# Performance work log

Hardware: AMD Instinct MI355X
Metric: run time of the kernel (lower is better)

Reference implementation:

```python
import jax, jax.numpy as jnp
import numpy as np

D_E = 100   # entity embedding dim
D_R = 100   # relation embedding dim
RANK = 40   # TR rank
N_ENT = 10000
N_REL = 50
B = 128
EPS = 1e-5  # torch BatchNorm1d default eps


def _bn(x, gamma, beta):
    # BatchNorm1d in training mode: biased batch statistics over the batch dim.
    mu = x.mean(axis=0)
    var = x.var(axis=0)  # ddof=0, matches torch normalization variance
    return gamma * (x - mu) * jax.lax.rsqrt(var + EPS) + beta


def _tr_to_tensor(f0, f1, f2, f3):
    # Tensor-ring reconstruction of W with ring trace; factors are [R, d, R].
    # Pairwise contraction keeps intermediates at [R, d, d, R] (256 MB max).
    A = jnp.einsum('aib,bjc->aijc', f0, f1)   # [R, d_r, d_e, R]
    C = jnp.einsum('ckd,dla->ckla', f2, f3)   # [R, d_e, d_e, R]
    return jnp.einsum('aijc,ckla->ijkl', A, C)  # [d_r, d_e, d_e, d_e]


def setup_inputs() -> dict:
    key = jax.random.key(0)
    ks = jax.random.split(key, 10)
    E_weight = 0.001 * jax.random.normal(ks[0], (N_ENT, D_E), dtype=jnp.float32)
    E_weight = E_weight.at[0].set(0.0)  # padding_idx=0
    R_weight = 0.001 * jax.random.normal(ks[1], (N_REL, D_R), dtype=jnp.float32)
    R_weight = R_weight.at[0].set(0.0)
    f0 = jax.random.normal(ks[2], (RANK, D_R, RANK), dtype=jnp.float32) * 0.05
    f1 = jax.random.normal(ks[3], (RANK, D_E, RANK), dtype=jnp.float32) * 0.05
    f2 = jax.random.normal(ks[4], (RANK, D_E, RANK), dtype=jnp.float32) * 0.05
    f3 = jax.random.normal(ks[5], (RANK, D_E, RANK), dtype=jnp.float32) * 0.05
    bnr_g = jnp.ones((D_R,), jnp.float32); bnr_b = jnp.zeros((D_R,), jnp.float32)
    bne_g = jnp.ones((D_E,), jnp.float32); bne_b = jnp.zeros((D_E,), jnp.float32)
    bnw_g = jnp.ones((D_E,), jnp.float32); bnw_b = jnp.zeros((D_E,), jnp.float32)
    r_idx = jax.random.randint(ks[6], (B,), 0, N_REL)
    e_idx1 = jax.random.randint(ks[7], (B,), 0, N_ENT)
    e_idx2 = jax.random.randint(ks[8], (B,), 0, N_ENT)
    return {
        'E_weight': E_weight, 'R_weight': R_weight,
        'f0': f0, 'f1': f1, 'f2': f2, 'f3': f3,
        'bnr_g': bnr_g, 'bnr_b': bnr_b,
        'bne_g': bne_g, 'bne_b': bne_b,
        'bnw_g': bnw_g, 'bnw_b': bnw_b,
        'r_idx': r_idx, 'e_idx1': e_idx1, 'e_idx2': e_idx2,
        'miss_ent_domain': 2,
    }


def reference(E_weight, R_weight, f0, f1, f2, f3,
              bnr_g, bnr_b, bne_g, bne_b, bnw_g, bnw_b,
              r_idx, e_idx1, e_idx2, miss_ent_domain):
    # Reconstruct the full TR tensor every call, as the module does.
    W = _tr_to_tensor(f0, f1, f2, f3)                  # [d_r, d_e, d_e, d_e]
    r = _bn(R_weight[r_idx], bnr_g, bnr_b)             # [B, d_r]
    W_mat = (r @ W.reshape(D_R, -1)).reshape(-1, D_E, D_E, D_E)  # [B, d_e^3]
    # Dropouts are identity here (deterministic / eval mode).
    e1 = _bn(E_weight[e_idx1], bne_g, bne_b)           # [B, d_e]
    e2 = _bn(E_weight[e_idx2], bne_g, bne_b)           # [B, d_e]
    labs = 'ijk'  # ary = 3
    out_lab = labs[miss_ent_domain - 1]
    eq = f'b{labs},' + ','.join(f'b{l}' for l in labs if l != out_lab) + f'->b{out_lab}'
    W_out = jnp.einsum(eq, W_mat, e1, e2)              # [B, d_e]
    W_out = _bn(W_out, bnw_g, bnw_b)
    scores = W_out @ E_weight.T                        # [B, N_ENT]
    pred = jax.nn.softmax(scores, axis=1)
    return (pred, W)
```

## Files before the change

kernel.cpp:

```cpp
#include <hip/hip_runtime.h>
#include <hip/hip_bf16.h>

#define DE 100
#define RK 40
#define NENT 10000
#define BATCH 128
#define KDIM 1600
#define MN 10000
#define PRED_SIZE (BATCH*NENT)

typedef __bf16 bf16x8 __attribute__((ext_vector_type(8)));
typedef float floatx4 __attribute__((ext_vector_type(4)));

static __device__ __forceinline__ unsigned short f2bf(float f) {
    unsigned int u = __builtin_bit_cast(unsigned int, f);
    unsigned int lsb = (u >> 16) & 1u;
    u += 0x7fffu + lsb;
    return (unsigned short)(u >> 16);
}

__global__ void prep_A_kernel(const float* __restrict__ f0, const float* __restrict__ f1,
                              unsigned short* __restrict__ Abf) {
    const int m = blockIdx.x;
    const int i = m / 100, j = m % 100;
    const int t = threadIdx.x;
    __shared__ __align__(16) float P[KDIM];
    __shared__ __align__(16) float Q[KDIM];
    for (int e = t; e < KDIM; e += 256) {
        const int u = e / 40, v = e % 40;
        P[e] = f0[u*4000 + i*40 + v];
        Q[e] = f1[u*4000 + j*40 + v];
    }
    __syncthreads();
    for (int o = t; o < 400; o += 256) {
        const int x  = o / 10;
        const int z4 = (o % 10) * 4;
        float a0=0.f, a1=0.f, a2=0.f, a3=0.f;
        #pragma unroll
        for (int y = 0; y < 40; ++y) {
            const float s = P[x*40 + y];
            const float4 q = *reinterpret_cast<const float4*>(&Q[y*40 + z4]);
            a0 += s*q.x; a1 += s*q.y; a2 += s*q.z; a3 += s*q.w;
        }
        ushort4 r;
        r.x = f2bf(a0); r.y = f2bf(a1); r.z = f2bf(a2); r.w = f2bf(a3);
        *reinterpret_cast<ushort4*>(&Abf[(size_t)m*KDIM + x*40 + z4]) = r;
    }
}

__global__ void prep_B_kernel(const float* __restrict__ f2, const float* __restrict__ f3,
                              unsigned short* __restrict__ Bbf) {
    const int n = blockIdx.x;
    const int k = n / 100, l = n % 100;
    const int t = threadIdx.x;
    __shared__ __align__(16) float P[KDIM];
    __shared__ __align__(16) float Q[KDIM];
    __shared__ __align__(16) float Rt[KDIM];
    for (int e = t; e < KDIM; e += 256) {
        const int u = e / 40, v = e % 40;
        P[e] = f2[u*4000 + k*40 + v];
        Q[e] = f3[u*4000 + l*40 + v];
    }
    __syncthreads();
    for (int o = t; o < 400; o += 256) {
        const int x  = o / 10;
        const int z4 = (o % 10) * 4;
        float a0=0.f, a1=0.f, a2=0.f, a3=0.f;
        #pragma unroll
        for (int y = 0; y < 40; ++y) {
            const float s = P[x*40 + y];
            const float4 q = *reinterpret_cast<const float4*>(&Q[y*40 + z4]);
            a0 += s*q.x; a1 += s*q.y; a2 += s*q.z; a3 += s*q.w;
        }
        Rt[x*40 + z4 + 0] = a0; Rt[x*40 + z4 + 1] = a1;
        Rt[x*40 + z4 + 2] = a2; Rt[x*40 + z4 + 3] = a3;
    }
    __syncthreads();
    for (int o = t; o < 400; o += 256) {
        const int a  = o / 10;
        const int c4 = (o % 10) * 4;
        ushort4 r;
        r.x = f2bf(Rt[(c4+0)*40 + a]);
        r.y = f2bf(Rt[(c4+1)*40 + a]);
        r.z = f2bf(Rt[(c4+2)*40 + a]);
        r.w = f2bf(Rt[(c4+3)*40 + a]);
        *reinterpret_cast<ushort4*>(&Bbf[(size_t)n*KDIM + a*40 + c4]) = r;
    }
}

typedef __attribute__((address_space(1))) void gvoid;
typedef __attribute__((address_space(3))) void lvoid;
static __device__ __forceinline__ void async_cp16(const void* g, void* l) {
    gvoid* gp = (gvoid*)(unsigned long long)g;
    lvoid* lp = (lvoid*)(unsigned int)(unsigned long long)l;
    __builtin_amdgcn_global_load_lds(gp, lp, 16, 0, 0);
}

__global__ __launch_bounds__(256) void gemm_kernel(const unsigned short* __restrict__ A,
                                                   const unsigned short* __restrict__ Bm,
                                                   float* __restrict__ W) {
    __shared__ __align__(16) unsigned short As[4096];
    __shared__ __align__(16) unsigned short Bs[4096];
    const int t = threadIdx.x;
    const int w = t >> 6, l = t & 63;
    const int wm = w >> 1, wn = w & 1;
    const int quad = l >> 4, lrow = l & 15;
    const int m0 = blockIdx.y * 128, n0 = blockIdx.x * 128;

    const int srow = t >> 2;
    const int scol = (t & 3) * 8;
    const int rA0 = (m0 + srow      < MN) ? (m0 + srow)      : (MN-1);
    const int rA1 = (m0 + 64 + srow < MN) ? (m0 + 64 + srow) : (MN-1);
    const int rB0 = (n0 + srow      < MN) ? (n0 + srow)      : (MN-1);
    const int rB1 = (n0 + 64 + srow < MN) ? (n0 + 64 + srow) : (MN-1);
    const unsigned short* gA0 = A  + (size_t)rA0*KDIM + scol;
    const unsigned short* gA1 = A  + (size_t)rA1*KDIM + scol;
    const unsigned short* gB0 = Bm + (size_t)rB0*KDIM + scol;
    const unsigned short* gB1 = Bm + (size_t)rB1*KDIM + scol;
    unsigned short* lA0 = &As[w*512];
    unsigned short* lA1 = &As[2048 + w*512];
    unsigned short* lB0 = &Bs[w*512];
    unsigned short* lB1 = &Bs[2048 + w*512];

    floatx4 acc[4][4] = {};

    for (int k0 = 0; k0 < KDIM; k0 += 32) {
        async_cp16(gA0 + k0, lA0);
        async_cp16(gA1 + k0, lA1);
        async_cp16(gB0 + k0, lB0);
        async_cp16(gB1 + k0, lB1);
        __syncthreads();
        bf16x8 af[4], bfv[4];
        #pragma unroll
        for (int mi = 0; mi < 4; ++mi)
            af[mi] = *reinterpret_cast<const bf16x8*>(&As[(wm*64 + mi*16 + lrow)*32 + quad*8]);
        #pragma unroll
        for (int ni = 0; ni < 4; ++ni)
            bfv[ni] = *reinterpret_cast<const bf16x8*>(&Bs[(wn*64 + ni*16 + lrow)*32 + quad*8]);
        #pragma unroll
        for (int mi = 0; mi < 4; ++mi) {
            #pragma unroll
            for (int ni = 0; ni < 4; ++ni)
                acc[mi][ni] = __builtin_amdgcn_mfma_f32_16x16x32_bf16(af[mi], bfv[ni], acc[mi][ni], 0, 0, 0);
        }
        __syncthreads();
    }

    #pragma unroll
    for (int mi = 0; mi < 4; ++mi) {
        #pragma unroll
        for (int ni = 0; ni < 4; ++ni) {
            #pragma unroll
            for (int reg = 0; reg < 4; ++reg) {
                const int rg = m0 + wm*64 + mi*16 + quad*4 + reg;
                const int cg = n0 + wn*64 + ni*16 + lrow;
                if (rg < MN && cg < MN)
                    W[(size_t)rg * MN + cg] = acc[mi][ni][reg];
            }
        }
    }
}

__global__ void bn_kernel(const float* __restrict__ src, const int* __restrict__ idx,
                          const float* __restrict__ gamma, const float* __restrict__ beta,
                          float* __restrict__ out) {
    const int f = blockIdx.x;
    const int b = threadIdx.x;
    __shared__ float red[BATCH];
    const int row = idx ? idx[b] : b;
    const float x = src[row*DE + f];
    red[b] = x; __syncthreads();
    for (int s = 64; s > 0; s >>= 1) { if (b < s) red[b] += red[b + s]; __syncthreads(); }
    const float mu = red[0] * (1.0f/BATCH);
    __syncthreads();
    const float d = x - mu;
    red[b] = d * d; __syncthreads();
    for (int s = 64; s > 0; s >>= 1) { if (b < s) red[b] += red[b + s]; __syncthreads(); }
    const float var = red[0] * (1.0f/BATCH);
    out[b*DE + f] = gamma[f] * d / sqrtf(var + 1e-5f) + beta[f];
}

__global__ void proj_kernel(const float* __restrict__ rb, const float* __restrict__ e1b,
                            const float* __restrict__ e2b,
                            const float* __restrict__ f0, const float* __restrict__ f1,
                            const float* __restrict__ f2, const float* __restrict__ f3,
                            float* __restrict__ wraw) {
    const int b = blockIdx.x, t = threadIdx.x;
    __shared__ float rv[DE], e1v[DE], e2v[DE];
    __shared__ float R0[KDIM], E1[KDIM], E2[KDIM], T[KDIM], S[KDIM];
    if (t < DE) { rv[t] = rb[b*DE+t]; e1v[t] = e1b[b*DE+t]; e2v[t] = e2b[b*DE+t]; }
    __syncthreads();
    for (int e = t; e < KDIM; e += 256) {
        const int u = e / 40, v = e % 40;
        const int base = u*4000 + v;
        float aR=0.f, aE1=0.f, aE2=0.f;
        for (int p = 0; p < DE; ++p) {
            aR  += rv[p]  * f0[base + p*40];
            aE1 += e1v[p] * f1[base + p*40];
            aE2 += e2v[p] * f3[base + p*40];
        }
        R0[e] = aR; E1[e] = aE1; E2[e] = aE2;
    }
    __syncthreads();
    for (int e = t; e < KDIM; e += 256) {
        const int a = e / 40, c = e % 40;
        float acc = 0.f;
        #pragma unroll
        for (int y = 0; y < 40; ++y) acc += R0[a*40+y] * E1[y*40+c];
        T[e] = acc;
    }
    __syncthreads();
    for (int e = t; e < KDIM; e += 256) {
        const int c = e / 40, d = e % 40;
        float acc = 0.f;
        #pragma unroll
        for (int y = 0; y < 40; ++y) acc += T[y*40+c] * E2[d*40+y];
        S[e] = acc;
    }
    __syncthreads();
    if (t < DE) {
        float acc = 0.f;
        for (int c = 0; c < 40; ++c) {
            #pragma unroll
            for (int d = 0; d < 40; ++d)
                acc += S[c*40+d] * f2[c*4000 + t*40 + d];
        }
        wraw[b*DE + t] = acc;
    }
}

__global__ void scores_kernel(const float* __restrict__ wbn, const float* __restrict__ E,
                              float* __restrict__ scores) {
    const int bx = blockIdx.x;
    const int b = bx >> 3, chunk = bx & 7;
    const int t = threadIdx.x;
    __shared__ __align__(16) float wsh[DE];
    if (t < DE) wsh[t] = wbn[b*DE + t];
    __syncthreads();
    const float4* wv = reinterpret_cast<const float4*>(wsh);
    const int n_end = (chunk + 1) * 1250;
    for (int n = chunk*1250 + t; n < n_end; n += 256) {
        const float4* er = reinterpret_cast<const float4*>(E + (size_t)n * DE);
        float acc = 0.f;
        #pragma unroll
        for (int q = 0; q < 25; ++q) {
            const float4 e4 = er[q], w4 = wv[q];
            acc += e4.x*w4.x + e4.y*w4.y + e4.z*w4.z + e4.w*w4.w;
        }
        scores[(size_t)b*NENT + n] = acc;
    }
}

__global__ void softmax_reduce_kernel(const float* __restrict__ scores,
                                      float* __restrict__ rmax, float* __restrict__ rsum) {
    const int b = blockIdx.x, t = threadIdx.x;
    __shared__ float red[256];
    const float* s = scores + (size_t)b*NENT;
    float m = -1e30f;
    for (int n = t; n < NENT; n += 256) m = fmaxf(m, s[n]);
    red[t] = m; __syncthreads();
    for (int st = 128; st > 0; st >>= 1) { if (t < st) red[t] = fmaxf(red[t], red[t+st]); __syncthreads(); }
    m = red[0]; __syncthreads();
    float sum = 0.f;
    for (int n = t; n < NENT; n += 256) sum += expf(s[n] - m);
    red[t] = sum; __syncthreads();
    for (int st = 128; st > 0; st >>= 1) { if (t < st) red[t] += red[t+st]; __syncthreads(); }
    if (t == 0) { rmax[b] = m; rsum[b] = red[0]; }
}

__global__ void pred_kernel(float* __restrict__ out, const float* __restrict__ rmax,
                            const float* __restrict__ rsum) {
    const int i = blockIdx.x*256 + threadIdx.x;
    const int b = i / NENT;
    out[i] = expf(out[i] - rmax[b]) / rsum[b];
}

extern "C" void kernel_launch(void* const* d_in, const int* in_sizes, int n_in,
                              void* d_out, int out_size, void* d_ws, size_t ws_size,
                              hipStream_t stream) {
    (void)in_sizes; (void)n_in; (void)out_size; (void)ws_size;
    const float* E    = (const float*)d_in[0];
    const float* Rw   = (const float*)d_in[1];
    const float* f0   = (const float*)d_in[2];
    const float* f1   = (const float*)d_in[3];
    const float* f2   = (const float*)d_in[4];
    const float* f3   = (const float*)d_in[5];
    const float* bnrg = (const float*)d_in[6];
    const float* bnrb = (const float*)d_in[7];
    const float* bneg = (const float*)d_in[8];
    const float* bneb = (const float*)d_in[9];
    const float* bnwg = (const float*)d_in[10];
    const float* bnwb = (const float*)d_in[11];
    const int* r_idx  = (const int*)d_in[12];
    const int* e_idx1 = (const int*)d_in[13];
    const int* e_idx2 = (const int*)d_in[14];

    float* out = (float*)d_out;
    float* Wt  = out + PRED_SIZE;

    char* ws = (char*)d_ws;
    unsigned short* Abf = (unsigned short*)ws;
    unsigned short* Bbf = (unsigned short*)(ws + 32000000);
    float* rbn  = (float*)(ws + 64000000);
    float* e1bn = rbn  + BATCH*DE;
    float* e2bn = e1bn + BATCH*DE;
    float* wraw = e2bn + BATCH*DE;
    float* wbn  = wraw + BATCH*DE;
    float* rmax = wbn  + BATCH*DE;
    float* rsum = rmax + BATCH;

    prep_A_kernel<<<MN, 256, 0, stream>>>(f0, f1, Abf);
    prep_B_kernel<<<MN, 256, 0, stream>>>(f2, f3, Bbf);
    gemm_kernel<<<dim3(79, 79), 256, 0, stream>>>(Abf, Bbf, Wt);

    bn_kernel<<<DE, BATCH, 0, stream>>>(Rw, r_idx, bnrg, bnrb, rbn);
    bn_kernel<<<DE, BATCH, 0, stream>>>(E, e_idx1, bneg, bneb, e1bn);
    bn_kernel<<<DE, BATCH, 0, stream>>>(E, e_idx2, bneg, bneb, e2bn);
    proj_kernel<<<BATCH, 256, 0, stream>>>(rbn, e1bn, e2bn, f0, f1, f2, f3, wraw);
    bn_kernel<<<DE, BATCH, 0, stream>>>(wraw, nullptr, bnwg, bnwb, wbn);
    scores_kernel<<<BATCH*8, 256, 0, stream>>>(wbn, E, out);
    softmax_reduce_kernel<<<BATCH, 256, 0, stream>>>(out, rmax, rsum);
    pred_kernel<<<PRED_SIZE/256, 256, 0, stream>>>(out, rmax, rsum);
}
```

Measured before the change: 1.367 ms.

## Restructure bf16 GEMM into 256x256 double-buffered tiles with swizzled LDS

The W-reconstruction GEMM moves from 128x128 tiles with single-buffered K=32 steps to 256x256 tiles on 512 threads. It uses K=64 steps, double-buffered async global-to-LDS copies, and an XOR-swizzled LDS layout to avoid bank conflicts. A block-index remap groups neighbouring tiles for better L2 reuse, and s_setprio raises priority around the MFMA bursts. The goal is more reuse per loaded byte and overlap of loads with MFMA work. The cost is 128KB of dynamic LDS per block, which limits occupancy to one block per CU and depends on the hand-written waitcnt and barrier sequencing being correct.

```diff
diff --git a/kernel.cpp b/kernel.cpp
--- a/kernel.cpp
+++ b/kernel.cpp
@@ -96,63 +96,113 @@
     __builtin_amdgcn_global_load_lds(gp, lp, 16, 0, 0);
 }
 
-__global__ __launch_bounds__(256) void gemm_kernel(const unsigned short* __restrict__ A,
-                                                   const unsigned short* __restrict__ Bm,
-                                                   float* __restrict__ W) {
-    __shared__ __align__(16) unsigned short As[4096];
-    __shared__ __align__(16) unsigned short Bs[4096];
+#define NKT 25
+#define LDS_TILE 16384
+
+__global__ __launch_bounds__(512, 2) void gemm_kernel(const unsigned short* __restrict__ A,
+                                                      const unsigned short* __restrict__ Bm,
+                                                      float* __restrict__ W) {
+    extern __shared__ unsigned short lds[];
     const int t = threadIdx.x;
     const int w = t >> 6, l = t & 63;
-    const int wm = w >> 1, wn = w & 1;
+    const int wm = w >> 2, wn = w & 3;
     const int quad = l >> 4, lrow = l & 15;
-    const int m0 = blockIdx.y * 128, n0 = blockIdx.x * 128;
-
-    const int srow = t >> 2;
-    const int scol = (t & 3) * 8;
-    const int rA0 = (m0 + srow      < MN) ? (m0 + srow)      : (MN-1);
-    const int rA1 = (m0 + 64 + srow < MN) ? (m0 + 64 + srow) : (MN-1);
-    const int rB0 = (n0 + srow      < MN) ? (n0 + srow)      : (MN-1);
-    const int rB1 = (n0 + 64 + srow < MN) ? (n0 + 64 + srow) : (MN-1);
-    const unsigned short* gA0 = A  + (size_t)rA0*KDIM + scol;
-    const unsigned short* gA1 = A  + (size_t)rA1*KDIM + scol;
-    const unsigned short* gB0 = Bm + (size_t)rB0*KDIM + scol;
-    const unsigned short* gB1 = Bm + (size_t)rB1*KDIM + scol;
-    unsigned short* lA0 = &As[w*512];
-    unsigned short* lA1 = &As[2048 + w*512];
-    unsigned short* lB0 = &Bs[w*512];
-    unsigned short* lB1 = &Bs[2048 + w*512];
-
-    floatx4 acc[4][4] = {};
-
-    for (int k0 = 0; k0 < KDIM; k0 += 32) {
-        async_cp16(gA0 + k0, lA0);
-        async_cp16(gA1 + k0, lA1);
-        async_cp16(gB0 + k0, lB0);
-        async_cp16(gB1 + k0, lB1);
-        __syncthreads();
-        bf16x8 af[4], bfv[4];
-        #pragma unroll
-        for (int mi = 0; mi < 4; ++mi)
-            af[mi] = *reinterpret_cast<const bf16x8*>(&As[(wm*64 + mi*16 + lrow)*32 + quad*8]);
-        #pragma unroll
-        for (int ni = 0; ni < 4; ++ni)
-            bfv[ni] = *reinterpret_cast<const bf16x8*>(&Bs[(wn*64 + ni*16 + lrow)*32 + quad*8]);
-        #pragma unroll
-        for (int mi = 0; mi < 4; ++mi) {
-            #pragma unroll
-            for (int ni = 0; ni < 4; ++ni)
-                acc[mi][ni] = __builtin_amdgcn_mfma_f32_16x16x32_bf16(af[mi], bfv[ni], acc[mi][ni], 0, 0, 0);
-        }
-        __syncthreads();
-    }
-
+    const int swz = lrow & 7;
+
+    const int orig = blockIdx.x;
+    const int sb = (orig & 7) * 200 + (orig >> 3);
+    const int by = sb / 40, bx = sb % 40;
+    const int m0 = by * 256, n0 = bx * 256;
+
+    const int srow = t >> 3;
+    const int schk = (t & 7) ^ (srow & 7);
+    int offA[4], offB[4];
     #pragma unroll
-    for (int mi = 0; mi < 4; ++mi) {
+    for (int i = 0; i < 4; ++i) {
+        int ra = m0 + i*64 + srow; if (ra > MN-1) ra = MN-1;
+        int rb = n0 + i*64 + srow; if (rb > MN-1) rb = MN-1;
+        offA[i] = ra * KDIM + schk * 8;
+        offB[i] = rb * KDIM + schk * 8;
+    }
+    const int lds_off = t * 8;
+
+    floatx4 acc[8][4] = {};
+
+    #pragma unroll
+    for (int i = 0; i < 4; ++i) {
+        async_cp16(A  + offA[i], lds + i*4096 + lds_off);
+        async_cp16(Bm + offB[i], lds + LDS_TILE + i*4096 + lds_off);
+    }
+
+    for (int kt = 0; kt < NKT; ++kt) {
+        const int cur = kt & 1;
+        const unsigned short* As = lds + cur * (2*LDS_TILE);
+        const unsigned short* Bs = As + LDS_TILE;
+
+        if (kt < NKT-1) {
+            unsigned short* An = lds + (cur ^ 1) * (2*LDS_TILE);
+            unsigned short* Bn = An + LDS_TILE;
+            const int koff = (kt + 1) * 64;
+            #pragma unroll
+            for (int i = 0; i < 4; ++i) {
+                async_cp16(A  + offA[i] + koff, An + i*4096 + lds_off);
+                async_cp16(Bm + offB[i] + koff, Bn + i*4096 + lds_off);
+            }
+            asm volatile("s_waitcnt vmcnt(8)" ::: "memory");
+        } else {
+            asm volatile("s_waitcnt vmcnt(0)" ::: "memory");
+        }
+        __builtin_amdgcn_s_barrier();
+        asm volatile("" ::: "memory");
+
+        bf16x8 b[4][2];
         #pragma unroll
         for (int ni = 0; ni < 4; ++ni) {
+            const int row = wn*64 + ni*16 + lrow;
+            #pragma unroll
+            for (int kk = 0; kk < 2; ++kk) {
+                const int ch = ((kk << 2) | quad) ^ swz;
+                b[ni][kk] = *reinterpret_cast<const bf16x8*>(&Bs[row*64 + ch*8]);
+            }
+        }
+        #pragma unroll
+        for (int mh = 0; mh < 2; ++mh) {
+            bf16x8 a[4][2];
+            #pragma unroll
+            for (int mi2 = 0; mi2 < 4; ++mi2) {
+                const int row = wm*128 + mh*64 + mi2*16 + lrow;
+                #pragma unroll
+                for (int kk = 0; kk < 2; ++kk) {
+                    const int ch = ((kk << 2) | quad) ^ swz;
+                    a[mi2][kk] = *reinterpret_cast<const bf16x8*>(&As[row*64 + ch*8]);
+                }
+            }
+            __builtin_amdgcn_s_setprio(1);
+            #pragma unroll
+            for (int mi2 = 0; mi2 < 4; ++mi2) {
+                #pragma unroll
+                for (int ni = 0; ni < 4; ++ni) {
+                    acc[mh*4+mi2][ni] = __builtin_amdgcn_mfma_f32_16x16x32_bf16(
+                        a[mi2][0], b[ni][0], acc[mh*4+mi2][ni], 0, 0, 0);
+                    acc[mh*4+mi2][ni] = __builtin_amdgcn_mfma_f32_16x16x32_bf16(
+                        a[mi2][1], b[ni][1], acc[mh*4+mi2][ni], 0, 0, 0);
+                }
+            }
+            __builtin_amdgcn_s_setprio(0);
+        }
+
+        asm volatile("s_waitcnt lgkmcnt(0)" ::: "memory");
+        __builtin_amdgcn_s_barrier();
+        asm volatile("" ::: "memory");
+    }
+
+    #pragma unroll
+    for (int mi = 0; mi < 8; ++mi) {
+        #pragma unroll
+        for (int ni = 0; ni < 4; ++ni) {
             #pragma unroll
             for (int reg = 0; reg < 4; ++reg) {
-                const int rg = m0 + wm*64 + mi*16 + quad*4 + reg;
+                const int rg = m0 + wm*128 + mi*16 + quad*4 + reg;
                 const int cg = n0 + wn*64 + ni*16 + lrow;
                 if (rg < MN && cg < MN)
                     W[(size_t)rg * MN + cg] = acc[mi][ni][reg];
@@ -309,9 +359,16 @@
     float* rmax = wbn  + BATCH*DE;
     float* rsum = rmax + BATCH;
 
+    static bool s_attr = false;
+    if (!s_attr) {
+        hipFuncSetAttribute((const void*)gemm_kernel,
+                            hipFuncAttributeMaxDynamicSharedMemorySize, 131072);
+        s_attr = true;
+    }
+
     prep_A_kernel<<<MN, 256, 0, stream>>>(f0, f1, Abf);
     prep_B_kernel<<<MN, 256, 0, stream>>>(f2, f3, Bbf);
-    gemm_kernel<<<dim3(79, 79), 256, 0, stream>>>(Abf, Bbf, Wt);
+    gemm_kernel<<<1600, 512, 131072, stream>>>(Abf, Bbf, Wt);
 
     bn_kernel<<<DE, BATCH, 0, stream>>>(Rw, r_idx, bnrg, bnrb, rbn);
     bn_kernel<<<DE, BATCH, 0, stream>>>(E, e_idx1, bneg, bneb, e1bn);
```

After: 1.161 ms. 1.18x faster.
